# Kernel tuning notes

Hardware: AMD Instinct MI355X
Metric: run time of the kernel (lower is better)

## Reference

```python
import jax, jax.numpy as jnp
import numpy as np

B, S, HID = 1, 2048, 2048
H, KV, D = 16, 8, 128          # heads, kv heads, head_dim
EPS = 1e-6
THETA_T, THETA_HW = 1000000.0, 10000.0
SCALE = D ** -0.5
NEG = -1e9


def _rms(x, w):
    xf = x.astype(jnp.float32)
    var = jnp.mean(xf * xf, axis=-1, keepdims=True)
    return (w * (xf * jax.lax.rsqrt(var + EPS))).astype(x.dtype)


def _rope_cs(pos, theta, half_dim):
    # Module builds RoPE with head_dim = 2*half_dim then takes every-other freq:
    # exponents arange(0, 2*half_dim, 4) / (2*half_dim)  -> half_dim//2 freqs
    dim2 = 2 * half_dim
    inv_freq = 1.0 / theta ** (jnp.arange(0, dim2, 4, dtype=jnp.float32) / dim2)
    freqs = pos.astype(jnp.float32)[:, None] * inv_freq[None, :]   # [S, half_dim//2]
    emb = jnp.concatenate([freqs, freqs], axis=-1)                 # [S, half_dim]
    return jnp.cos(emb), jnp.sin(emb)


def _rot_half(x):
    d = x.shape[-1] // 2
    return jnp.concatenate([-x[..., d:], x[..., :d]], axis=-1)


def _apply_rope(q, k, cos, sin):
    cos = cos[None, None]  # [1,1,S,dim]
    sin = sin[None, None]
    return q * cos + _rot_half(q) * sin, k * cos + _rot_half(k) * sin


def setup_inputs() -> dict:
    key = jax.random.key(0)
    ks = jax.random.split(key, 10)
    hidden_states = jax.random.normal(ks[0], (B, S, HID), jnp.float32)
    indexes = jax.random.randint(ks[1], (3, S), 0, S)
    causal = jnp.tril(jnp.ones((S, S), bool))
    attention_mask = jnp.where(causal, 0.0, NEG).astype(jnp.float32)[None, None]
    qkv_w = jax.random.normal(ks[2], ((H + 2 * KV) * D, HID), jnp.float32) * 0.02
    qkv_b = jax.random.normal(ks[3], ((H + 2 * KV) * D,), jnp.float32) * 0.02
    o_w = jax.random.normal(ks[4], (HID, H * D), jnp.float32) * 0.02
    o_b = jax.random.normal(ks[5], (HID,), jnp.float32) * 0.02
    q_norm_w = jnp.ones((D // 2,), jnp.float32)
    k_norm_w = jnp.ones((D // 2,), jnp.float32)
    q_norm_hw_w = jnp.ones((D // 2,), jnp.float32)
    k_norm_hw_w = jnp.ones((D // 2,), jnp.float32)
    return dict(hidden_states=hidden_states, indexes=indexes, attention_mask=attention_mask,
                qkv_w=qkv_w, qkv_b=qkv_b, o_w=o_w, o_b=o_b,
                q_norm_w=q_norm_w, k_norm_w=k_norm_w,
                q_norm_hw_w=q_norm_hw_w, k_norm_hw_w=k_norm_hw_w)


def reference(hidden_states, indexes, attention_mask, qkv_w, qkv_b, o_w, o_b,
              q_norm_w, k_norm_w, q_norm_hw_w, k_norm_hw_w):
    b, s, _ = hidden_states.shape
    qkv = hidden_states @ qkv_w.T + qkv_b
    q, k, v = jnp.split(qkv, [H * D, H * D + KV * D], axis=-1)
    q = q.reshape(b, s, H, D)
    k = k.reshape(b, s, KV, D)
    v = v.reshape(b, s, KV, D)

    # split head_dim into time half and hw half
    q_t, q_hw = jnp.split(q, 2, axis=-1)
    k_t, k_hw = jnp.split(k, 2, axis=-1)
    q_t = jnp.swapaxes(_rms(q_t, q_norm_w), 1, 2)       # [B,H,S,D/2]
    k_t = jnp.swapaxes(_rms(k_t, k_norm_w), 1, 2)
    q_hw = jnp.swapaxes(_rms(q_hw, q_norm_hw_w), 1, 2)
    k_hw = jnp.swapaxes(_rms(k_hw, k_norm_hw_w), 1, 2)
    q_h, q_ww = jnp.split(q_hw, 2, axis=-1)             # [B,H,S,D/4]
    k_h, k_ww = jnp.split(k_hw, 2, axis=-1)

    cos_t, sin_t = _rope_cs(indexes[0], THETA_T, D // 2)
    q_t, k_t = _apply_rope(q_t, k_t, cos_t, sin_t)
    cos_h, sin_h = _rope_cs(indexes[1], THETA_HW, D // 4)
    q_h, k_h = _apply_rope(q_h, k_h, cos_h, sin_h)
    cos_w, sin_w = _rope_cs(indexes[2], THETA_HW, D // 4)
    q_ww, k_ww = _apply_rope(q_ww, k_ww, cos_w, sin_w)

    query = jnp.concatenate([q_t, q_h, q_ww], axis=-1)  # [B,H,S,D]
    keyst = jnp.concatenate([k_t, k_h, k_ww], axis=-1)  # [B,KV,S,D]
    value = jnp.swapaxes(v, 1, 2)                       # [B,KV,S,D]

    n_rep = H // KV
    keyst = jnp.repeat(keyst, n_rep, axis=1)
    value = jnp.repeat(value, n_rep, axis=1)

    scores = jnp.einsum('bhsd,bhtd->bhst', query, keyst) * SCALE + attention_mask
    probs = jax.nn.softmax(scores.astype(jnp.float32), axis=-1).astype(query.dtype)
    attn = jnp.einsum('bhst,bhtd->bhsd', probs, value)
    attn = jnp.swapaxes(attn, 1, 2).reshape(b, s, H * D)
    return attn @ o_w.T + o_b
```

## Files before the change

### kernel.cpp

```cpp
#include <hip/hip_runtime.h>

typedef __bf16 bf16;
typedef __bf16 bf16x4 __attribute__((ext_vector_type(4)));
typedef __bf16 bf16x8 __attribute__((ext_vector_type(8)));
typedef float f32x4 __attribute__((ext_vector_type(4)));

#define S_LEN 2048
#define HIDDEN 2048
#define NH 16
#define NKV 8
#define HD 128
#define QKV_N 4096

#define PSLOT 66560

__device__ __forceinline__ void async_load16(const void* g, void* l) {
  __builtin_amdgcn_global_load_lds((const __attribute__((address_space(1))) unsigned int*)g,
                                   (__attribute__((address_space(3))) unsigned int*)l,
                                   16, 0, 0);
}

template <int C>
__device__ __forceinline__ float dpp_f(float x) {
  return __builtin_bit_cast(float, __builtin_amdgcn_mov_dpp(
      __builtin_bit_cast(int, x), C, 0xF, 0xF, true));
}
__device__ __forceinline__ float rowmax16(float x) {
  x = fmaxf(x, dpp_f<0x128>(x));
  x = fmaxf(x, dpp_f<0x124>(x));
  x = fmaxf(x, dpp_f<0x122>(x));
  x = fmaxf(x, dpp_f<0x121>(x));
  return x;
}
__device__ __forceinline__ float rowsum16(float x) {
  x += dpp_f<0x128>(x);
  x += dpp_f<0x124>(x);
  x += dpp_f<0x122>(x);
  x += dpp_f<0x121>(x);
  return x;
}

__global__ __launch_bounds__(256)
void cvt_f32_bf16(const float* __restrict__ src, bf16* __restrict__ dst, int n) {
  int i = (blockIdx.x * 256 + threadIdx.x) * 4;
  if (i < n) {
    float4 v = *(const float4*)(src + i);
    bf16x4 o = {(bf16)v.x, (bf16)v.y, (bf16)v.z, (bf16)v.w};
    *(bf16x4*)(dst + i) = o;
  }
}

__global__ __launch_bounds__(256)
void cvt_pair(const float* __restrict__ s1, bf16* __restrict__ d1, int n1,
              const float* __restrict__ s2, bf16* __restrict__ d2, int n2) {
  int i = (blockIdx.x * 256 + threadIdx.x) * 4;
  const float* s;
  bf16* d;
  int j;
  if (i < n1) { s = s1; d = d1; j = i; }
  else        { s = s2; d = d2; j = i - n1; if (j >= n2) return; }
  float4 v = *(const float4*)(s + j);
  bf16x4 o = {(bf16)v.x, (bf16)v.y, (bf16)v.z, (bf16)v.w};
  *(bf16x4*)(d + j) = o;
}

template <int WRITE_BF16>
__global__ __launch_bounds__(256)
void gemm_bt(const bf16* __restrict__ A, const bf16* __restrict__ B,
             const float* __restrict__ bias, void* __restrict__ Cout,
             int M, int N, int K) {
  __shared__ bf16 As[2][128 * 32];
  __shared__ bf16 Bs[2][128 * 32];
  const int tid = threadIdx.x;
  const int w = tid >> 6, lane = tid & 63;
  const int quad = lane >> 4, l15 = lane & 15;
  const int wm = w >> 1, wn = w & 1;

  const int flat = blockIdx.y * gridDim.x + blockIdx.x;
  const int xcd = flat & 7, loc = flat >> 3;
  const int colsPer = gridDim.x >> 3;
  const int nidx = xcd * colsPer + loc / gridDim.y;
  const int midx = loc % gridDim.y;
  const int m0 = midx * 128, n0 = nidx * 128;

  f32x4 acc[4][4];
#pragma unroll
  for (int i = 0; i < 4; i++)
#pragma unroll
    for (int j = 0; j < 4; j++) acc[i][j] = (f32x4){0.f, 0.f, 0.f, 0.f};

  const int crow = lane >> 2;
  const int ccol = (lane & 3) * 8;

#pragma unroll
  for (int q = 0; q < 2; q++) {
    int c = 2 * w + q;
    async_load16(A + (size_t)(m0 + c * 16 + crow) * K + ccol, (char*)As[0] + c * 1024);
    async_load16(B + (size_t)(n0 + c * 16 + crow) * K + ccol, (char*)Bs[0] + c * 1024);
  }

  int cur = 0;
  for (int k0 = 0; k0 < K; k0 += 32) {
    __asm__ __volatile__("s_waitcnt vmcnt(0)" ::: "memory");
    __syncthreads();
    if (k0 + 32 < K) {
#pragma unroll
      for (int q = 0; q < 2; q++) {
        int c = 2 * w + q;
        async_load16(A + (size_t)(m0 + c * 16 + crow) * K + k0 + 32 + ccol,
                     (char*)As[cur ^ 1] + c * 1024);
        async_load16(B + (size_t)(n0 + c * 16 + crow) * K + k0 + 32 + ccol,
                     (char*)Bs[cur ^ 1] + c * 1024);
      }
    }
    bf16x8 af[4], bfr[4];
#pragma unroll
    for (int i = 0; i < 4; i++)
      af[i] = *(const bf16x8*)(As[cur] + (wm * 64 + i * 16 + l15) * 32 + quad * 8);
#pragma unroll
    for (int j = 0; j < 4; j++)
      bfr[j] = *(const bf16x8*)(Bs[cur] + (wn * 64 + j * 16 + l15) * 32 + quad * 8);
#pragma unroll
    for (int i = 0; i < 4; i++)
#pragma unroll
      for (int j = 0; j < 4; j++)
        acc[i][j] = __builtin_amdgcn_mfma_f32_16x16x32_bf16(af[i], bfr[j], acc[i][j], 0, 0, 0);
    cur ^= 1;
  }

#pragma unroll
  for (int i = 0; i < 4; i++) {
#pragma unroll
    for (int j = 0; j < 4; j++) {
      int col = n0 + wn * 64 + j * 16 + l15;
      float bv = bias[col];
#pragma unroll
      for (int r = 0; r < 4; r++) {
        int row = m0 + wm * 64 + i * 16 + quad * 4 + r;
        float v = acc[i][j][r] + bv;
        if (WRITE_BF16)
          ((bf16*)Cout)[(size_t)row * N + col] = (bf16)v;
        else
          ((float*)Cout)[(size_t)row * N + col] = v;
      }
    }
  }
}

__global__ __launch_bounds__(128)
void normrope(const bf16* __restrict__ qkv, const int* __restrict__ idx,
              const float* __restrict__ qnw, const float* __restrict__ knw,
              const float* __restrict__ qnhw, const float* __restrict__ knhw,
              bf16* __restrict__ Qb, bf16* __restrict__ Kb) {
  const int s = blockIdx.x;
  const int y = blockIdx.y;
  const int d = threadIdx.x;

  const bool isq = (y < 16);
  const int off = isq ? (y * HD + d) : (2048 + (y - 16) * HD + d);
  float x = (float)qkv[(size_t)s * QKV_N + off];

  float ss = x * x;
#pragma unroll
  for (int o = 32; o; o >>= 1) ss += __shfl_xor(ss, o);
  float inv = rsqrtf(ss * (1.f / 64.f) + 1e-6f);
  const float* wt = (d < 64) ? (isq ? qnw : knw) : (isq ? qnhw : knhw);
  float yn = x * inv * wt[d & 63];

  float pos, invf;
  int xorm;
  bool firsthalf;
  if (d < 64) {
    pos = (float)idx[s];
    int i = d & 31;
    invf = exp2f(-(float)i * 0.6228615177913804f);
    xorm = 32;
    firsthalf = (d < 32);
  } else {
    int j = d - 64;
    int region = j >> 5;
    pos = (float)idx[(1 + region) * S_LEN + s];
    int i = j & 15;
    invf = exp2f(-(float)i * 0.8304820237218406f);
    xorm = 16;
    firsthalf = ((j & 31) < 16);
  }
  float ang = pos * invf;
  float si, co;
  sincosf(ang, &si, &co);
  float partner = __shfl_xor(yn, xorm);
  float outv = firsthalf ? (yn * co - partner * si) : (yn * co + partner * si);

  if (isq)
    Qb[((size_t)y * S_LEN + s) * HD + d] = (bf16)(outv * 0.12751745f);
  else
    Kb[((size_t)(y - 16) * S_LEN + s) * HD + d] = (bf16)outv;
}

__global__ __launch_bounds__(256)
void vtrans(const bf16* __restrict__ qkv, bf16* __restrict__ VT) {
  __shared__ bf16 T[64][72];
  const int tid = threadIdx.x;
  const int s0 = blockIdx.x * 64, d0 = blockIdx.y * 64, kv = blockIdx.z;
#pragma unroll
  for (int it = 0; it < 2; it++) {
    int r = (tid >> 3) + it * 32;
    int c = (tid & 7) * 8;
    bf16x8 v = *(const bf16x8*)(qkv + (size_t)(s0 + r) * QKV_N + 3072 + kv * HD + d0 + c);
    *(bf16x8*)(&T[r][c]) = v;
  }
  __syncthreads();
#pragma unroll
  for (int it = 0; it < 2; it++) {
    int r = (tid >> 3) + it * 32;
    int c = (tid & 7) * 8;
    bf16x8 o;
#pragma unroll
    for (int j = 0; j < 8; j++) o[j] = T[c + j][r];
    *(bf16x8*)(VT + ((size_t)kv * HD + d0 + r) * S_LEN + s0 + c) = o;
  }
}

__global__ __launch_bounds__(256)
void attn_fused(const bf16* __restrict__ Qb, const bf16* __restrict__ Kb,
                const bf16* __restrict__ VT, bf16* __restrict__ attnO,
                char* __restrict__ Opart) {
  __shared__ bf16 Kbuf[2][8192];
  __shared__ bf16 Vbuf[8192];
  __shared__ __align__(16) bf16 Ps[4][2][16][72];
  const int tid = threadIdx.x;
  const int w = tid >> 6, lane = tid & 63;
  const int quad = lane >> 4, l15 = lane & 15;
  const int b = blockIdx.x;
  const int h = b & 15;
  const int cid = b >> 4;
  int G, c, nc;
  if (cid < 7)       { G = cid;          c = 0;     nc = 1; }
  else if (cid < 21) { int t = cid - 7;  G = 7 + (t >> 1);  c = t & 1; nc = 2; }
  else               { int t = cid - 21; G = 14 + t / 3;    c = t % 3; nc = 3; }
  const int nT = 2 * G + 2;
  const int tBeg = c * 14;
  const int tEnd = (tBeg + 14 < nT) ? (tBeg + 14) : nT;
  const int tCap0 = 2 * G + 1;
  const int kv = h >> 1;
  const int qr0h[2] = {G * 128 + w * 16, G * 128 + 64 + w * 16};

  const bf16* Qg = Qb + (size_t)h * S_LEN * HD;
  const bf16* Kg = Kb + (size_t)kv * S_LEN * HD;
  const bf16* Vg = VT + (size_t)kv * HD * S_LEN;

  const bf16* ksrc = Kg + (size_t)(w * 16 + l15) * HD + quad * 8;
  const bf16* vsrc = Vg + (size_t)(2 * w * 16 + l15) * S_LEN + quad * 8;

  bf16x8 aq[2][4];
#pragma unroll
  for (int bb = 0; bb < 2; bb++)
#pragma unroll
    for (int kc = 0; kc < 4; kc++)
      aq[bb][kc] = *(const bf16x8*)(Qg + (size_t)(qr0h[bb] + l15) * HD + kc * 32 + quad * 8);

  float m2[2][4], li[2][4];
  f32x4 Oacc[2][8];
#pragma unroll
  for (int bb = 0; bb < 2; bb++) {
#pragma unroll
    for (int r = 0; r < 4; r++) { m2[bb][r] = -1e30f; li[bb][r] = 0.f; }
#pragma unroll
    for (int dt = 0; dt < 8; dt++) Oacc[bb][dt] = (f32x4){0.f, 0.f, 0.f, 0.f};
  }

#pragma unroll
  for (int kc = 0; kc < 4; kc++)
    async_load16(ksrc + (size_t)(tBeg << 6) * HD + kc * 32,
                 (char*)Kbuf[tBeg & 1] + (w * 4 + kc) * 1024);

  for (int tt = tBeg; tt < tEnd; ++tt) {
    const int t0 = tt << 6;
    const int cur = tt & 1;
    const bool more = (tt + 1 < tEnd);
    const bool do0 = (tt < tCap0);
    __asm__ __volatile__("s_waitcnt vmcnt(0)" ::: "memory");
    __syncthreads();

#pragma unroll
    for (int e = 0; e < 2; e++)
#pragma unroll
      for (int half = 0; half < 2; half++)
        async_load16(vsrc + (size_t)e * 16 * S_LEN + t0 + half * 32,
                     (char*)Vbuf + (half * 8 + 2 * w + e) * 1024);
    if (more) {
#pragma unroll
      for (int kc = 0; kc < 4; kc++)
        async_load16(ksrc + (size_t)(t0 + 64) * HD + kc * 32,
                     (char*)Kbuf[cur ^ 1] + (w * 4 + kc) * 1024);
    }

#pragma unroll
    for (int bb = 0; bb < 2; bb++) {
      if (bb == 0 && !do0) continue;
      const int qr0 = qr0h[bb];
      f32x4 sacc[4];
#pragma unroll
      for (int nt = 0; nt < 4; nt++) {
        sacc[nt] = (f32x4){0.f, 0.f, 0.f, 0.f};
#pragma unroll
        for (int kc = 0; kc < 4; kc++) {
          bf16x8 bk = *(const bf16x8*)((const char*)Kbuf[cur] + (nt * 4 + kc) * 1024 + lane * 16);
          sacc[nt] = __builtin_amdgcn_mfma_f32_16x16x32_bf16(aq[bb][kc], bk, sacc[nt], 0, 0, 0);
        }
      }
      const bool full = (t0 + 64 <= qr0);
      float mxv[4];
      bool need = false;
#pragma unroll
      for (int r = 0; r < 4; r++) {
        if (!full) {
          const int mrow = qr0 + quad * 4 + r;
          const int cb = t0 + l15;
          if (cb > mrow) sacc[0][r] = -1e30f;
          if (cb + 16 > mrow) sacc[1][r] = -1e30f;
          if (cb + 32 > mrow) sacc[2][r] = -1e30f;
          if (cb + 48 > mrow) sacc[3][r] = -1e30f;
        }
        mxv[r] = rowmax16(fmaxf(fmaxf(sacc[0][r], sacc[1][r]), fmaxf(sacc[2][r], sacc[3][r])));
        need = need || (mxv[r] > m2[bb][r] + 8.f);
      }
      if (__any(need ? 1 : 0)) {
#pragma unroll
        for (int r = 0; r < 4; r++) {
          float mnew = fmaxf(m2[bb][r], mxv[r]);
          float a = exp2f(m2[bb][r] - mnew);
          li[bb][r] *= a;
#pragma unroll
          for (int dt = 0; dt < 8; dt++) Oacc[bb][dt][r] *= a;
          m2[bb][r] = mnew;
        }
      }
#pragma unroll
      for (int r = 0; r < 4; r++) {
        float p0 = exp2f(sacc[0][r] - m2[bb][r]);
        float p1 = exp2f(sacc[1][r] - m2[bb][r]);
        float p2 = exp2f(sacc[2][r] - m2[bb][r]);
        float p3 = exp2f(sacc[3][r] - m2[bb][r]);
        li[bb][r] += rowsum16((p0 + p1) + (p2 + p3));
        Ps[w][bb][quad * 4 + r][l15] = (bf16)p0;
        Ps[w][bb][quad * 4 + r][16 + l15] = (bf16)p1;
        Ps[w][bb][quad * 4 + r][32 + l15] = (bf16)p2;
        Ps[w][bb][quad * 4 + r][48 + l15] = (bf16)p3;
      }
    }
    __asm__ __volatile__("s_waitcnt lgkmcnt(0)" ::: "memory");
    if (more)
      __asm__ __volatile__("s_waitcnt vmcnt(4)" ::: "memory");
    else
      __asm__ __volatile__("s_waitcnt vmcnt(0)" ::: "memory");

#pragma unroll
    for (int bb = 0; bb < 2; bb++) {
      if (bb == 0 && !do0) continue;
#pragma unroll
      for (int half = 0; half < 2; half++) {
        bf16x8 ap = *(const bf16x8*)(&Ps[w][bb][l15][half * 32 + quad * 8]);
#pragma unroll
        for (int dt = 0; dt < 8; dt++) {
          bf16x8 bv = *(const bf16x8*)((const char*)Vbuf + (half * 8 + dt) * 1024 + lane * 16);
          Oacc[bb][dt] = __builtin_amdgcn_mfma_f32_16x16x32_bf16(ap, bv, Oacc[bb][dt], 0, 0, 0);
        }
      }
    }
  }

  if (nc > 1) {
    char* slot = Opart + (size_t)((cid - 7) * 16 + h) * PSLOT;
    float* Op = (float*)slot;
    float* mlp = (float*)(slot + 65536);
#pragma unroll
    for (int bb = 0; bb < 2; bb++) {
#pragma unroll
      for (int r = 0; r < 4; r++) {
        const int row = bb * 64 + w * 16 + quad * 4 + r;
#pragma unroll
        for (int dt = 0; dt < 8; dt++)
          Op[row * 128 + dt * 16 + l15] = Oacc[bb][dt][r];
        if (l15 == 0) {
          mlp[row * 2 + 0] = m2[bb][r];
          mlp[row * 2 + 1] = li[bb][r];
        }
      }
    }
  } else {
#pragma unroll
    for (int bb = 0; bb < 2; bb++) {
#pragma unroll
      for (int r = 0; r < 4; r++) {
        float invl = 1.f / li[bb][r];
        int srow = qr0h[bb] + quad * 4 + r;
#pragma unroll
        for (int dt = 0; dt < 8; dt++)
          attnO[(size_t)srow * HIDDEN + h * HD + dt * 16 + l15] = (bf16)(Oacc[bb][dt][r] * invl);
      }
    }
  }
}

__global__ __launch_bounds__(256)
void attn_merge(const char* __restrict__ Opart, bf16* __restrict__ attnO) {
  const int h = blockIdx.x & 15;
  const int idx = blockIdx.x >> 4;
  int G, nc, cid0;
  if (idx < 7) { G = 7 + idx;        nc = 2; cid0 = 7 + idx * 2; }
  else         { G = 14 + (idx - 7); nc = 3; cid0 = 21 + (idx - 7) * 3; }
  const char* s0 = Opart + (size_t)((cid0 - 7) * 16 + h) * PSLOT;
  const char* s1 = s0 + (size_t)16 * PSLOT;
  const char* s2 = s0 + (size_t)32 * PSLOT;
  const float* O0 = (const float*)s0;
  const float* O1 = (const float*)s1;
  const float* O2 = (const float*)s2;
  const float* ML0 = (const float*)(s0 + 65536);
  const float* ML1 = (const float*)(s1 + 65536);
  const float* ML2 = (const float*)(s2 + 65536);
  const int t = threadIdx.x;
#pragma unroll
  for (int it = 0; it < 16; ++it) {
    int e = it * 256 + t;
    int row = e >> 5, d = (e & 31) * 4;
    float m0 = ML0[row * 2], l0 = ML0[row * 2 + 1];
    float m1 = ML1[row * 2], l1 = ML1[row * 2 + 1];
    float m2v = -1e30f, l2v = 0.f;
    if (nc == 3) { m2v = ML2[row * 2]; l2v = ML2[row * 2 + 1]; }
    float m = fmaxf(fmaxf(m0, m1), m2v);
    float a0 = exp2f(m0 - m), a1 = exp2f(m1 - m), a2 = exp2f(m2v - m);
    float inv = 1.f / (a0 * l0 + a1 * l1 + a2 * l2v);
    f32x4 x0 = *(const f32x4*)(O0 + row * 128 + d);
    f32x4 x1 = *(const f32x4*)(O1 + row * 128 + d);
    f32x4 x2 = (f32x4){0.f, 0.f, 0.f, 0.f};
    if (nc == 3) x2 = *(const f32x4*)(O2 + row * 128 + d);
    int srow = G * 128 + row;
    bf16x4 o;
#pragma unroll
    for (int j = 0; j < 4; j++)
      o[j] = (bf16)((a0 * x0[j] + a1 * x1[j] + a2 * x2[j]) * inv);
    *(bf16x4*)(attnO + (size_t)srow * HIDDEN + h * HD + d) = o;
  }
}

extern "C" void kernel_launch(void* const* d_in, const int* in_sizes, int n_in,
                              void* d_out, int out_size, void* d_ws, size_t ws_size,
                              hipStream_t stream) {
  const float* hidden = (const float*)d_in[0];
  const int* idx = (const int*)d_in[1];
  const float* qkv_w = (const float*)d_in[3];
  const float* qkv_b = (const float*)d_in[4];
  const float* o_w = (const float*)d_in[5];
  const float* o_b = (const float*)d_in[6];
  const float* qnw = (const float*)d_in[7];
  const float* knw = (const float*)d_in[8];
  const float* qnhw = (const float*)d_in[9];
  const float* knhw = (const float*)d_in[10];

  char* ws = (char*)d_ws;
  bf16* hB    = (bf16*)(ws);
  bf16* qwB   = (bf16*)(ws + (8u << 20));
  bf16* qkvB  = (bf16*)(ws + (24u << 20));
  bf16* Qb    = (bf16*)(ws + (40u << 20));
  bf16* Kb    = (bf16*)(ws + (48u << 20));
  bf16* VT    = (bf16*)(ws + (52u << 20));
  bf16* owB   = hB;
  char* Opart = ws + (8u << 20);
  bf16* attn  = (bf16*)(ws + (32u << 20));

  cvt_pair<<<12288, 256, 0, stream>>>(hidden, hB, HIDDEN * S_LEN,
                                      qkv_w, qwB, QKV_N * HIDDEN);

  gemm_bt<1><<<dim3(QKV_N / 128, S_LEN / 128), 256, 0, stream>>>(
      hB, qwB, qkv_b, qkvB, S_LEN, QKV_N, HIDDEN);

  cvt_f32_bf16<<<HIDDEN * HIDDEN / 1024, 256, 0, stream>>>(o_w, owB, HIDDEN * HIDDEN);

  normrope<<<dim3(S_LEN, 24), 128, 0, stream>>>(qkvB, idx, qnw, knw, qnhw, knhw, Qb, Kb);
  vtrans<<<dim3(S_LEN / 64, HD / 64, NKV), 256, 0, stream>>>(qkvB, VT);

  attn_fused<<<432, 256, 0, stream>>>(Qb, Kb, VT, attn, Opart);
  attn_merge<<<144, 256, 0, stream>>>(Opart, attn);

  gemm_bt<0><<<dim3(HIDDEN / 128, S_LEN / 128), 256, 0, stream>>>(
      attn, owB, o_b, (float*)d_out, S_LEN, HIDDEN, HIDDEN);
}
```

Baseline: 317.0 us.

## Deepen GEMM K-tile, drop XCD swizzle, batch rows per normrope block

The GEMM now stages a 64-wide K slice per iteration with a chunked LDS layout, which halves the number of barrier/waitcnt rounds and doubles the MFMA work between syncs. The XCD-aware block remapping is removed in favour of plain blockIdx mapping. normrope processes 8 sequence rows per block, hoisting the weights and RoPE frequencies and cutting the launch grid eightfold. This trades higher LDS usage (64KB per GEMM block), which may lower occupancy, and possibly worse L2 locality without the swizzle.

```diff
diff --git a/kernel.cpp b/kernel.cpp
--- a/kernel.cpp
+++ b/kernel.cpp
@@ -69,19 +69,13 @@
 void gemm_bt(const bf16* __restrict__ A, const bf16* __restrict__ B,
              const float* __restrict__ bias, void* __restrict__ Cout,
              int M, int N, int K) {
-  __shared__ bf16 As[2][128 * 32];
-  __shared__ bf16 Bs[2][128 * 32];
+  __shared__ bf16 As[2][128 * 64];
+  __shared__ bf16 Bs[2][128 * 64];
   const int tid = threadIdx.x;
   const int w = tid >> 6, lane = tid & 63;
   const int quad = lane >> 4, l15 = lane & 15;
   const int wm = w >> 1, wn = w & 1;
-
-  const int flat = blockIdx.y * gridDim.x + blockIdx.x;
-  const int xcd = flat & 7, loc = flat >> 3;
-  const int colsPer = gridDim.x >> 3;
-  const int nidx = xcd * colsPer + loc / gridDim.y;
-  const int midx = loc % gridDim.y;
-  const int m0 = midx * 128, n0 = nidx * 128;
+  const int m0 = blockIdx.y * 128, n0 = blockIdx.x * 128;
 
   f32x4 acc[4][4];
 #pragma unroll
@@ -93,38 +87,49 @@
   const int ccol = (lane & 3) * 8;
 
 #pragma unroll
-  for (int q = 0; q < 2; q++) {
-    int c = 2 * w + q;
-    async_load16(A + (size_t)(m0 + c * 16 + crow) * K + ccol, (char*)As[0] + c * 1024);
-    async_load16(B + (size_t)(n0 + c * 16 + crow) * K + ccol, (char*)Bs[0] + c * 1024);
+  for (int q = 0; q < 4; q++) {
+    int c = w * 4 + q, rb = c >> 1, kh = c & 1;
+    async_load16(A + (size_t)(m0 + rb * 16 + crow) * K + kh * 32 + ccol,
+                 (char*)As[0] + c * 1024);
+    async_load16(B + (size_t)(n0 + rb * 16 + crow) * K + kh * 32 + ccol,
+                 (char*)Bs[0] + c * 1024);
   }
 
   int cur = 0;
-  for (int k0 = 0; k0 < K; k0 += 32) {
+  for (int k0 = 0; k0 < K; k0 += 64) {
     __asm__ __volatile__("s_waitcnt vmcnt(0)" ::: "memory");
     __syncthreads();
-    if (k0 + 32 < K) {
-#pragma unroll
-      for (int q = 0; q < 2; q++) {
-        int c = 2 * w + q;
-        async_load16(A + (size_t)(m0 + c * 16 + crow) * K + k0 + 32 + ccol,
+    if (k0 + 64 < K) {
+#pragma unroll
+      for (int q = 0; q < 4; q++) {
+        int c = w * 4 + q, rb = c >> 1, kh = c & 1;
+        async_load16(A + (size_t)(m0 + rb * 16 + crow) * K + k0 + 64 + kh * 32 + ccol,
                      (char*)As[cur ^ 1] + c * 1024);
-        async_load16(B + (size_t)(n0 + c * 16 + crow) * K + k0 + 32 + ccol,
+        async_load16(B + (size_t)(n0 + rb * 16 + crow) * K + k0 + 64 + kh * 32 + ccol,
                      (char*)Bs[cur ^ 1] + c * 1024);
       }
     }
-    bf16x8 af[4], bfr[4];
+    bf16x8 af[4][2], bfr[4][2];
 #pragma unroll
     for (int i = 0; i < 4; i++)
-      af[i] = *(const bf16x8*)(As[cur] + (wm * 64 + i * 16 + l15) * 32 + quad * 8);
+#pragma unroll
+      for (int kk = 0; kk < 2; kk++)
+        af[i][kk] = *(const bf16x8*)((const char*)As[cur] +
+                                     ((wm * 4 + i) * 2 + kk) * 1024 + l15 * 64 + quad * 16);
 #pragma unroll
     for (int j = 0; j < 4; j++)
-      bfr[j] = *(const bf16x8*)(Bs[cur] + (wn * 64 + j * 16 + l15) * 32 + quad * 8);
-#pragma unroll
-    for (int i = 0; i < 4; i++)
-#pragma unroll
-      for (int j = 0; j < 4; j++)
-        acc[i][j] = __builtin_amdgcn_mfma_f32_16x16x32_bf16(af[i], bfr[j], acc[i][j], 0, 0, 0);
+#pragma unroll
+      for (int kk = 0; kk < 2; kk++)
+        bfr[j][kk] = *(const bf16x8*)((const char*)Bs[cur] +
+                                      ((wn * 4 + j) * 2 + kk) * 1024 + l15 * 64 + quad * 16);
+#pragma unroll
+    for (int kk = 0; kk < 2; kk++)
+#pragma unroll
+      for (int i = 0; i < 4; i++)
+#pragma unroll
+        for (int j = 0; j < 4; j++)
+          acc[i][j] = __builtin_amdgcn_mfma_f32_16x16x32_bf16(af[i][kk], bfr[j][kk],
+                                                              acc[i][j], 0, 0, 0);
     cur ^= 1;
   }
 
@@ -152,49 +157,56 @@
               const float* __restrict__ qnw, const float* __restrict__ knw,
               const float* __restrict__ qnhw, const float* __restrict__ knhw,
               bf16* __restrict__ Qb, bf16* __restrict__ Kb) {
-  const int s = blockIdx.x;
   const int y = blockIdx.y;
   const int d = threadIdx.x;
 
   const bool isq = (y < 16);
   const int off = isq ? (y * HD + d) : (2048 + (y - 16) * HD + d);
-  float x = (float)qkv[(size_t)s * QKV_N + off];
-
-  float ss = x * x;
-#pragma unroll
-  for (int o = 32; o; o >>= 1) ss += __shfl_xor(ss, o);
-  float inv = rsqrtf(ss * (1.f / 64.f) + 1e-6f);
   const float* wt = (d < 64) ? (isq ? qnw : knw) : (isq ? qnhw : knhw);
-  float yn = x * inv * wt[d & 63];
-
-  float pos, invf;
-  int xorm;
+  const float wv = wt[d & 63];
+
+  float invf;
+  int xorm, posrow;
   bool firsthalf;
   if (d < 64) {
-    pos = (float)idx[s];
     int i = d & 31;
     invf = exp2f(-(float)i * 0.6228615177913804f);
     xorm = 32;
     firsthalf = (d < 32);
+    posrow = 0;
   } else {
     int j = d - 64;
     int region = j >> 5;
-    pos = (float)idx[(1 + region) * S_LEN + s];
     int i = j & 15;
     invf = exp2f(-(float)i * 0.8304820237218406f);
     xorm = 16;
     firsthalf = ((j & 31) < 16);
-  }
-  float ang = pos * invf;
-  float si, co;
-  sincosf(ang, &si, &co);
-  float partner = __shfl_xor(yn, xorm);
-  float outv = firsthalf ? (yn * co - partner * si) : (yn * co + partner * si);
-
-  if (isq)
-    Qb[((size_t)y * S_LEN + s) * HD + d] = (bf16)(outv * 0.12751745f);
-  else
-    Kb[((size_t)(y - 16) * S_LEN + s) * HD + d] = (bf16)outv;
+    posrow = 1 + region;
+  }
+
+  bf16* outp = isq ? (Qb + ((size_t)y * S_LEN) * HD + d)
+                   : (Kb + ((size_t)(y - 16) * S_LEN) * HD + d);
+  const float oscale = isq ? 0.12751745f : 1.0f;
+
+#pragma unroll
+  for (int si = 0; si < 8; si++) {
+    const int s = blockIdx.x * 8 + si;
+    float x = (float)qkv[(size_t)s * QKV_N + off];
+
+    float ss = x * x;
+#pragma unroll
+    for (int o = 32; o; o >>= 1) ss += __shfl_xor(ss, o);
+    float inv = rsqrtf(ss * (1.f / 64.f) + 1e-6f);
+    float yn = x * inv * wv;
+
+    float pos = (float)idx[posrow * S_LEN + s];
+    float ang = pos * invf;
+    float si_, co;
+    sincosf(ang, &si_, &co);
+    float partner = __shfl_xor(yn, xorm);
+    float outv = firsthalf ? (yn * co - partner * si_) : (yn * co + partner * si_);
+    outp[(size_t)s * HD] = (bf16)(outv * oscale);
+  }
 }
 
 __global__ __launch_bounds__(256)
@@ -477,7 +489,7 @@
 
   cvt_f32_bf16<<<HIDDEN * HIDDEN / 1024, 256, 0, stream>>>(o_w, owB, HIDDEN * HIDDEN);
 
-  normrope<<<dim3(S_LEN, 24), 128, 0, stream>>>(qkvB, idx, qnw, knw, qnhw, knhw, Qb, Kb);
+  normrope<<<dim3(S_LEN / 8, 24), 128, 0, stream>>>(qkvB, idx, qnw, knw, qnhw, knhw, Qb, Kb);
   vtrans<<<dim3(S_LEN / 64, HD / 64, NKV), 256, 0, stream>>>(qkvB, VT);
 
   attn_fused<<<432, 256, 0, stream>>>(Qb, Kb, VT, attn, Opart);
```

New measurement: 300.5 us. -5.2%, faster.
